# Kernel tuning notes

Measured on AMD Instinct MI355X. Metric: run time of the kernel, lower is better.

The kernel has to match this reference:

```python
import jax, jax.numpy as jnp
import numpy as np
from jax import lax

N_EXPERTS = 256
N_GROUP = 8
TOPK_GROUP = 4
TOP_K = 8
AUX_ALPHA = 0.001


def setup_inputs() -> dict:
    key = jax.random.key(0)
    k1, k2 = jax.random.split(key)
    hidden_states = jax.random.normal(k1, (16384, 2048), dtype=jnp.float32)
    weight = jax.random.normal(k2, (N_EXPERTS, 2048), dtype=jnp.float32) * 0.02
    return {"hidden_states": hidden_states, "weight": weight}


def reference(hidden_states, weight):
    n_tokens = hidden_states.shape[0]
    group_size = N_EXPERTS // N_GROUP  # 32

    # gating logits: [N, E]
    logits = jnp.einsum('nh,eh->ne', hidden_states, weight)

    # group-restricted top-k: [N, G, group_size] -> top TOPK_GROUP per group
    group_logits = logits.reshape(n_tokens, N_GROUP, group_size)
    gw, gi = lax.top_k(group_logits, TOPK_GROUP)          # [N, G, tg]
    gw = gw.reshape(n_tokens, N_GROUP * TOPK_GROUP)
    gi = gi.reshape(n_tokens, N_GROUP * TOPK_GROUP)

    # global top-k over the pooled group winners
    topk_weights, ti = lax.top_k(gw, TOP_K)               # [N, K]
    selected_group = ti // TOPK_GROUP
    expert_in_group = jnp.take_along_axis(gi, ti, axis=1)
    topk_idx = selected_group * group_size + expert_in_group  # [N, K]

    # norm_topk_prob=True
    topk_weights = topk_weights / (jnp.sum(topk_weights, axis=-1, keepdims=True) + 1e-20)

    # auxiliary load-balancing loss (training path)
    expert_mask = jax.nn.one_hot(topk_idx.reshape(-1), N_EXPERTS, dtype=jnp.float32)
    expert_counts = expert_mask.mean(axis=0)              # [E]
    expert_probs = jax.nn.softmax(logits, axis=-1).mean(axis=0)  # [E]
    aux_loss = jnp.sum(expert_counts * expert_probs) * AUX_ALPHA

    return topk_idx, topk_weights, aux_loss
```

## Files before the change

kernel.cpp:

```cpp
#include <hip/hip_runtime.h>
#include <math.h>

#define NTOK 16384
#define KD   2048
#define NE   256
#define BM   32
#define NSTEP 64
#define EPS  2.5e-4f

using bf16x8 = __attribute__((ext_vector_type(8))) short;
using f32x16 = __attribute__((ext_vector_type(16))) float;
using u16 = unsigned short;
using u32 = unsigned int;

__device__ __forceinline__ u16 f2bf(float x) {
    u32 u = __float_as_uint(x);
    return (u16)((u + 0x7FFFu + ((u >> 16) & 1u)) >> 16);
}
__device__ __forceinline__ float bf2f(u16 h) {
    return __uint_as_float(((u32)h) << 16);
}

__global__ __launch_bounds__(256) void wsplit_kernel(
    const float* __restrict__ wgt, u16* __restrict__ Whi, u16* __restrict__ Wlo)
{
    const int idx = blockIdx.x * 256 + threadIdx.x;
    const int e  = idx >> 8;
    const int ko = idx & 255;
    const int k  = ko * 8;
    const int c  = k >> 5, s = (k >> 4) & 1, kh = (k >> 3) & 1;
    const int dst = (c * 2 + s) * 4096 + (e >> 6) * 1024 + ((e >> 5) & 1) * 512
                  + kh * 256 + (e & 31) * 8;
    const float* p = wgt + (size_t)e * KD + k;
    u16 hi[8], lo[8];
#pragma unroll
    for (int i = 0; i < 8; ++i) {
        const float w = p[i];
        hi[i] = f2bf(w);
        lo[i] = f2bf(w - bf2f(hi[i]));
    }
    *(uint4*)(Whi + dst) = *(const uint4*)hi;
    *(uint4*)(Wlo + dst) = *(const uint4*)lo;
}

__global__ __launch_bounds__(256, 4) void gate_kernel(
    const float* __restrict__ hid, const u16* __restrict__ Whi, const u16* __restrict__ Wlo,
    float* __restrict__ out, float* __restrict__ cnt, float* __restrict__ prb,
    int* __restrict__ flagcnt, int* __restrict__ flaglist)
{
    __shared__ union {
        struct { u16 ah[2][BM][40]; u16 al[2][BM][40]; } st;
        float ls[BM][257];
    } sh;
    __shared__ float maxS[BM], sumS[BM], invS[BM];

    const int tid  = threadIdx.x;
    const int lane = tid & 63;
    const int wv   = tid >> 6;
    const int ln31 = lane & 31;
    const int kh8  = (lane >> 5) * 8;
    const int t0   = blockIdx.x * BM;

    f32x16 acc[2];
#pragma unroll
    for (int nf = 0; nf < 2; ++nf)
#pragma unroll
        for (int r = 0; r < 16; ++r) acc[nf][r] = 0.f;

    float4 areg;
    const int am = tid >> 3;
    const int ak = (tid & 7) * 4;

    auto loadA = [&](int c) {
        areg = *(const float4*)(hid + (size_t)(t0 + am) * KD + c * 32 + ak);
    };
    auto writeA = [&](int buf) {
        float f[4] = {areg.x, areg.y, areg.z, areg.w};
#pragma unroll
        for (int i = 0; i < 4; ++i) {
            const u16 hi = f2bf(f[i]);
            sh.st.ah[buf][am][ak + i] = hi;
            sh.st.al[buf][am][ak + i] = f2bf(f[i] - bf2f(hi));
        }
    };

    loadA(0); writeA(0);
    int cur = 0;

#pragma unroll 1
    for (int c = 0; c < NSTEP; ++c) {
        __syncthreads();
        const int nxt = cur ^ 1;
        if (c + 1 < NSTEP) loadA(c + 1);

        const u16* bbase = (const u16*)0;
#pragma unroll
        for (int s = 0; s < 2; ++s) {
            const int boff = (c * 2 + s) * 4096 + wv * 1024 + lane * 8;
            const bf16x8 bh0 = *(const bf16x8*)(Whi + boff);
            const bf16x8 bl0 = *(const bf16x8*)(Wlo + boff);
            const bf16x8 bh1 = *(const bf16x8*)(Whi + boff + 512);
            const bf16x8 bl1 = *(const bf16x8*)(Wlo + boff + 512);
            const bf16x8 ah  = *(const bf16x8*)&sh.st.ah[cur][ln31][s * 16 + kh8];
            const bf16x8 al  = *(const bf16x8*)&sh.st.al[cur][ln31][s * 16 + kh8];

            acc[0] = __builtin_amdgcn_mfma_f32_32x32x16_bf16(ah, bh0, acc[0], 0, 0, 0);
            acc[0] = __builtin_amdgcn_mfma_f32_32x32x16_bf16(ah, bl0, acc[0], 0, 0, 0);
            acc[0] = __builtin_amdgcn_mfma_f32_32x32x16_bf16(al, bh0, acc[0], 0, 0, 0);
            acc[1] = __builtin_amdgcn_mfma_f32_32x32x16_bf16(ah, bh1, acc[1], 0, 0, 0);
            acc[1] = __builtin_amdgcn_mfma_f32_32x32x16_bf16(ah, bl1, acc[1], 0, 0, 0);
            acc[1] = __builtin_amdgcn_mfma_f32_32x32x16_bf16(al, bh1, acc[1], 0, 0, 0);
        }
        (void)bbase;
        if (c + 1 < NSTEP) writeA(nxt);
        cur = nxt;
    }

    __syncthreads();
#pragma unroll
    for (int nf = 0; nf < 2; ++nf) {
        const int col = wv * 64 + nf * 32 + ln31;
#pragma unroll
        for (int r = 0; r < 16; ++r) {
            const int row = (r & 3) + 8 * (r >> 2) + 4 * (lane >> 5);
            sh.ls[row][col] = acc[nf][r];
        }
    }
    if (tid < BM) sumS[tid] = 0.f;
    __syncthreads();

    if (tid < BM) {
        const float* lr = &sh.ls[tid][0];
        float tv[9]; int ti[9];
#pragma unroll
        for (int j = 0; j < 9; ++j) { tv[j] = -1e30f; ti[j] = 0; }
        float gv3[8], gv4[8];
        float rowmax = -1e30f;

        auto ins9 = [&](float v, int idx) {
#pragma unroll
            for (int p = 0; p < 9; ++p) {
                if (v > tv[p]) {
#pragma unroll
                    for (int q = 8; q > p; --q) { tv[q] = tv[q - 1]; ti[q] = ti[q - 1]; }
                    tv[p] = v; ti[p] = idx;
                    break;
                }
            }
        };

#pragma unroll 1
        for (int g = 0; g < 8; ++g) {
            float v0 = -1e30f, v1 = -1e30f, v2 = -1e30f, v3 = -1e30f, v4 = -1e30f;
            int   i0 = 0, i1 = 0, i2 = 0, i3 = 0;
            for (int j = 0; j < 32; ++j) {
                const float v = lr[g * 32 + j];
                if (v > v0)      { v4=v3; v3=v2;i3=i2; v2=v1;i2=i1; v1=v0;i1=i0; v0=v;i0=j; }
                else if (v > v1) { v4=v3; v3=v2;i3=i2; v2=v1;i2=i1; v1=v;i1=j; }
                else if (v > v2) { v4=v3; v3=v2;i3=i2; v2=v;i2=j; }
                else if (v > v3) { v4=v3; v3=v;i3=j; }
                else if (v > v4) { v4=v; }
            }
            rowmax = fmaxf(rowmax, v0);
            gv3[g] = v3; gv4[g] = v4;
            ins9(v0, g * 32 + i0);
            ins9(v1, g * 32 + i1);
            ins9(v2, g * 32 + i2);
            ins9(v3, g * 32 + i3);
        }

        bool flag = false;
#pragma unroll
        for (int r = 0; r < 8; ++r)
            if (tv[r] - tv[r + 1] < EPS) flag = true;
#pragma unroll
        for (int g = 0; g < 8; ++g)
            if (gv3[g] - gv4[g] < EPS && gv3[g] > tv[7] - EPS) flag = true;

        const float s01 = __fadd_rn(tv[0], tv[1]);
        const float s23 = __fadd_rn(tv[2], tv[3]);
        const float s45 = __fadd_rn(tv[4], tv[5]);
        const float s67 = __fadd_rn(tv[6], tv[7]);
        float s = __fadd_rn(__fadd_rn(s01, s23), __fadd_rn(s45, s67));
        s = __fadd_rn(s, 1e-20f);

        const size_t tg2 = (size_t)(t0 + tid);
#pragma unroll
        for (int j = 0; j < 8; ++j) {
            out[tg2 * 8 + j]                    = (float)ti[j];
            out[(size_t)NTOK * 8 + tg2 * 8 + j] = __fdiv_rn(tv[j], s);
            atomicAdd(&cnt[ti[j]], 1.0f);
        }
        if (flag) {
            const int fi = atomicAdd(flagcnt, 1);
            flaglist[fi] = t0 + tid;
        }
        maxS[tid] = rowmax;
    }
    __syncthreads();

    {
        const int t  = tid >> 3;
        const int c0 = (tid & 7) * 32;
        const float m = maxS[t];
        float part = 0.f;
#pragma unroll
        for (int j = 0; j < 32; ++j) part += __expf(sh.ls[t][c0 + j] - m);
        atomicAdd(&sumS[t], part);
    }
    __syncthreads();
    if (tid < BM) invS[tid] = 1.0f / sumS[tid];
    __syncthreads();

    {
        float p = 0.f;
#pragma unroll
        for (int n = 0; n < BM; ++n) p += __expf(sh.ls[n][tid] - maxS[n]) * invS[n];
        atomicAdd(&prb[tid], p);
    }
}

__global__ __launch_bounds__(256) void exact_kernel(
    const float* __restrict__ hid, const float* __restrict__ wgt,
    float* __restrict__ out, float* __restrict__ cnt,
    const int* __restrict__ flagcnt, const int* __restrict__ flaglist)
{
    const int fn = *flagcnt;

    __shared__ float wch[256 * 17];
    __shared__ float hch[8 * 17];
    __shared__ float exls[8][257];
    __shared__ int tk[8];

    const int tid = threadIdx.x;
    const int tg  = tid >> 7;
    const int eg  = (tid >> 2) & 31;
    const int l   = tid & 3;

#pragma unroll 1
    for (int base = blockIdx.x * 8; base < fn; base += 64 * 8) {
        const int nt = min(8, fn - base);
        __syncthreads();
        if (tid < 8) tk[tid] = (tid < nt) ? flaglist[base + tid] : flaglist[base];
        __syncthreads();

        float accq[4][8];
#pragma unroll
        for (int i = 0; i < 4; ++i)
#pragma unroll
            for (int j = 0; j < 8; ++j) accq[i][j] = 0.f;

#pragma unroll 1
        for (int c = 0; c < 128; ++c) {
            __syncthreads();
            {
                const float* p = wgt + (size_t)tid * KD + c * 16;
                float4 w0 = *(const float4*)(p);
                float4 w1 = *(const float4*)(p + 4);
                float4 w2 = *(const float4*)(p + 8);
                float4 w3 = *(const float4*)(p + 12);
                float* wr = &wch[tid * 17];
                wr[0]=w0.x; wr[1]=w0.y; wr[2]=w0.z; wr[3]=w0.w;
                wr[4]=w1.x; wr[5]=w1.y; wr[6]=w1.z; wr[7]=w1.w;
                wr[8]=w2.x; wr[9]=w2.y; wr[10]=w2.z; wr[11]=w2.w;
                wr[12]=w3.x; wr[13]=w3.y; wr[14]=w3.z; wr[15]=w3.w;
            }
            if (tid < 128) {
                const int tok = tid >> 4, k = tid & 15;
                hch[tok * 17 + k] = hid[(size_t)tk[tok] * KD + c * 16 + k];
            }
            __syncthreads();

#pragma unroll
            for (int q = 3; q >= 0; --q) {
                const int k = 4 * q + l;
                float hv[4], wv2[8];
#pragma unroll
                for (int i = 0; i < 4; ++i) hv[i] = hch[(tg * 4 + i) * 17 + k];
#pragma unroll
                for (int j = 0; j < 8; ++j) wv2[j] = wch[(j * 32 + eg) * 17 + k];
#pragma unroll
                for (int i = 0; i < 4; ++i)
#pragma unroll
                    for (int j = 0; j < 8; ++j)
                        accq[i][j] = __fadd_rn(__fmul_rn(hv[i], wv2[j]), accq[i][j]);
            }
        }

        __syncthreads();
#pragma unroll
        for (int i = 0; i < 4; ++i)
#pragma unroll
            for (int j = 0; j < 8; ++j) {
                float v = accq[i][j];
                v = __fadd_rn(v, __shfl_xor(v, 1));
                v = __fadd_rn(v, __shfl_xor(v, 2));
                if (l == 0) exls[tg * 4 + i][j * 32 + eg] = v;
            }
        __syncthreads();

        if (tid < nt) {
            const float* lr = &exls[tid][0];
            float tv[8]; int ti[8];
#pragma unroll
            for (int j = 0; j < 8; ++j) { tv[j] = -1e30f; ti[j] = 0; }

            auto ins8 = [&](float v, int idx) {
#pragma unroll
                for (int p = 0; p < 8; ++p) {
                    if (v > tv[p]) {
#pragma unroll
                        for (int q = 7; q > p; --q) { tv[q] = tv[q - 1]; ti[q] = ti[q - 1]; }
                        tv[p] = v; ti[p] = idx;
                        break;
                    }
                }
            };

#pragma unroll 1
            for (int g = 0; g < 8; ++g) {
                float v0 = -1e30f, v1 = -1e30f, v2 = -1e30f, v3 = -1e30f;
                int   i0 = 0, i1 = 0, i2 = 0, i3 = 0;
                for (int j = 0; j < 32; ++j) {
                    const float v = lr[g * 32 + j];
                    if (v > v0)      { v3=v2;i3=i2; v2=v1;i2=i1; v1=v0;i1=i0; v0=v;i0=j; }
                    else if (v > v1) { v3=v2;i3=i2; v2=v1;i2=i1; v1=v;i1=j; }
                    else if (v > v2) { v3=v2;i3=i2; v2=v;i2=j; }
                    else if (v > v3) { v3=v;i3=j; }
                }
                ins8(v0, g * 32 + i0);
                ins8(v1, g * 32 + i1);
                ins8(v2, g * 32 + i2);
                ins8(v3, g * 32 + i3);
            }

            const float s01 = __fadd_rn(tv[0], tv[1]);
            const float s23 = __fadd_rn(tv[2], tv[3]);
            const float s45 = __fadd_rn(tv[4], tv[5]);
            const float s67 = __fadd_rn(tv[6], tv[7]);
            float s = __fadd_rn(__fadd_rn(s01, s23), __fadd_rn(s45, s67));
            s = __fadd_rn(s, 1e-20f);

            const size_t gt = (size_t)tk[tid];
#pragma unroll
            for (int j = 0; j < 8; ++j) {
                const int oldi = (int)out[gt * 8 + j];
                if (oldi != ti[j]) {
                    atomicAdd(&cnt[oldi], -1.0f);
                    atomicAdd(&cnt[ti[j]], 1.0f);
                }
                out[gt * 8 + j]                    = (float)ti[j];
                out[(size_t)NTOK * 8 + gt * 8 + j] = __fdiv_rn(tv[j], s);
            }
        }
        __syncthreads();
    }
}

__global__ void aux_kernel(const float* __restrict__ cnt,
                           const float* __restrict__ prb,
                           float* __restrict__ out)
{
    const int tid = threadIdx.x;
    float v = cnt[tid] * prb[tid];
#pragma unroll
    for (int off = 32; off; off >>= 1) v += __shfl_down(v, off, 64);
    __shared__ float ps[4];
    if ((tid & 63) == 0) ps[tid >> 6] = v;
    __syncthreads();
    if (tid == 0) {
        const float tot = ps[0] + ps[1] + ps[2] + ps[3];
        out[(size_t)NTOK * 8 * 2] = tot * (0.001f / (131072.0f * 16384.0f));
    }
}

extern "C" void kernel_launch(void* const* d_in, const int* in_sizes, int n_in,
                              void* d_out, int out_size, void* d_ws, size_t ws_size,
                              hipStream_t stream)
{
    (void)in_sizes; (void)n_in; (void)out_size; (void)ws_size;
    const float* hid = (const float*)d_in[0];
    const float* wgt = (const float*)d_in[1];
    float* out = (float*)d_out;

    float* cnt      = (float*)d_ws;
    float* prb      = cnt + NE;
    int*   flagcnt  = (int*)(prb + NE);
    int*   flaglist = flagcnt + 64;
    u16*   Whi      = (u16*)(flaglist + NTOK);
    u16*   Wlo      = Whi + (size_t)NE * KD;

    hipMemsetAsync(d_ws, 0, (2 * NE + 64) * sizeof(float), stream);
    wsplit_kernel<<<NE * KD / 8 / 256, 256, 0, stream>>>(wgt, Whi, Wlo);
    gate_kernel<<<NTOK / BM, 256, 0, stream>>>(hid, Whi, Wlo, out, cnt, prb, flagcnt, flaglist);
    exact_kernel<<<64, 256, 0, stream>>>(hid, wgt, out, cnt, flagcnt, flaglist);
    aux_kernel<<<1, 256, 0, stream>>>(cnt, prb, out);
}
```

Baseline: 493.2 us.

## Register double-buffer weight fragments and unroll gate GEMM loop by two

The gate GEMM loop now prefetches the next chunk's bf16 hi/lo weight fragments into a second register set before issuing the current chunk's MFMAs. The loop is unrolled by two with fixed shared-memory buffer indices, so global weight loads overlap with matrix math rather than being issued and consumed back to back. The occupancy hint in launch_bounds is dropped so the compiler can use more registers for the extra fragments, which may reduce waves per CU. The exact kernel's grid stride now uses gridDim.x instead of a hardcoded 64.

```diff
diff --git a/kernel.cpp b/kernel.cpp
--- a/kernel.cpp
+++ b/kernel.cpp
@@ -43,7 +43,9 @@
     *(uint4*)(Wlo + dst) = *(const uint4*)lo;
 }
 
-__global__ __launch_bounds__(256, 4) void gate_kernel(
+#define MFMA32(A, B, C) __builtin_amdgcn_mfma_f32_32x32x16_bf16((A), (B), (C), 0, 0, 0)
+
+__global__ __launch_bounds__(256) void gate_kernel(
     const float* __restrict__ hid, const u16* __restrict__ Whi, const u16* __restrict__ Wlo,
     float* __restrict__ out, float* __restrict__ cnt, float* __restrict__ prb,
     int* __restrict__ flagcnt, int* __restrict__ flaglist)
@@ -84,39 +86,65 @@
         }
     };
 
-    loadA(0); writeA(0);
-    int cur = 0;
+    const u16* bwh = Whi + wv * 1024 + lane * 8;
+    const u16* bwl = Wlo + wv * 1024 + lane * 8;
+
+    bf16x8 p0h0, p0l0, p0h1, p0l1, p0h2, p0l2, p0h3, p0l3;
+    bf16x8 p1h0, p1l0, p1h1, p1l1, p1h2, p1l2, p1h3, p1l3;
+
+#define LOADB(P, cc) do {                                           \
+    const u16* _ph = bwh + (cc) * 8192;                             \
+    const u16* _pl = bwl + (cc) * 8192;                             \
+    P##h0 = *(const bf16x8*)(_ph);                                  \
+    P##l0 = *(const bf16x8*)(_pl);                                  \
+    P##h1 = *(const bf16x8*)(_ph + 512);                            \
+    P##l1 = *(const bf16x8*)(_pl + 512);                            \
+    P##h2 = *(const bf16x8*)(_ph + 4096);                           \
+    P##l2 = *(const bf16x8*)(_pl + 4096);                           \
+    P##h3 = *(const bf16x8*)(_ph + 4608);                           \
+    P##l3 = *(const bf16x8*)(_pl + 4608);                           \
+} while (0)
+
+#define COMPUTE(P, CUR) do {                                        \
+    bf16x8 ah0 = *(const bf16x8*)&sh.st.ah[CUR][ln31][kh8];         \
+    bf16x8 al0 = *(const bf16x8*)&sh.st.al[CUR][ln31][kh8];         \
+    acc[0] = MFMA32(ah0, P##h0, acc[0]);                            \
+    acc[0] = MFMA32(ah0, P##l0, acc[0]);                            \
+    acc[0] = MFMA32(al0, P##h0, acc[0]);                            \
+    acc[1] = MFMA32(ah0, P##h1, acc[1]);                            \
+    acc[1] = MFMA32(ah0, P##l1, acc[1]);                            \
+    acc[1] = MFMA32(al0, P##h1, acc[1]);                            \
+    bf16x8 ah1 = *(const bf16x8*)&sh.st.ah[CUR][ln31][16 + kh8];    \
+    bf16x8 al1 = *(const bf16x8*)&sh.st.al[CUR][ln31][16 + kh8];    \
+    acc[0] = MFMA32(ah1, P##h2, acc[0]);                            \
+    acc[0] = MFMA32(ah1, P##l2, acc[0]);                            \
+    acc[0] = MFMA32(al1, P##h2, acc[0]);                            \
+    acc[1] = MFMA32(ah1, P##h3, acc[1]);                            \
+    acc[1] = MFMA32(ah1, P##l3, acc[1]);                            \
+    acc[1] = MFMA32(al1, P##h3, acc[1]);                            \
+} while (0)
+
+    loadA(0);
+    writeA(0);
+    LOADB(p0, 0);
+    __syncthreads();
 
 #pragma unroll 1
-    for (int c = 0; c < NSTEP; ++c) {
-        __syncthreads();
-        const int nxt = cur ^ 1;
-        if (c + 1 < NSTEP) loadA(c + 1);
-
-        const u16* bbase = (const u16*)0;
-#pragma unroll
-        for (int s = 0; s < 2; ++s) {
-            const int boff = (c * 2 + s) * 4096 + wv * 1024 + lane * 8;
-            const bf16x8 bh0 = *(const bf16x8*)(Whi + boff);
-            const bf16x8 bl0 = *(const bf16x8*)(Wlo + boff);
-            const bf16x8 bh1 = *(const bf16x8*)(Whi + boff + 512);
-            const bf16x8 bl1 = *(const bf16x8*)(Wlo + boff + 512);
-            const bf16x8 ah  = *(const bf16x8*)&sh.st.ah[cur][ln31][s * 16 + kh8];
-            const bf16x8 al  = *(const bf16x8*)&sh.st.al[cur][ln31][s * 16 + kh8];
-
-            acc[0] = __builtin_amdgcn_mfma_f32_32x32x16_bf16(ah, bh0, acc[0], 0, 0, 0);
-            acc[0] = __builtin_amdgcn_mfma_f32_32x32x16_bf16(ah, bl0, acc[0], 0, 0, 0);
-            acc[0] = __builtin_amdgcn_mfma_f32_32x32x16_bf16(al, bh0, acc[0], 0, 0, 0);
-            acc[1] = __builtin_amdgcn_mfma_f32_32x32x16_bf16(ah, bh1, acc[1], 0, 0, 0);
-            acc[1] = __builtin_amdgcn_mfma_f32_32x32x16_bf16(ah, bl1, acc[1], 0, 0, 0);
-            acc[1] = __builtin_amdgcn_mfma_f32_32x32x16_bf16(al, bh1, acc[1], 0, 0, 0);
-        }
-        (void)bbase;
-        if (c + 1 < NSTEP) writeA(nxt);
-        cur = nxt;
-    }
-
-    __syncthreads();
+    for (int c = 0; c < NSTEP; c += 2) {
+        loadA(c + 1);
+        LOADB(p1, c + 1);
+        COMPUTE(p0, 0);
+        writeA(1);
+        __syncthreads();
+        if (c + 2 < NSTEP) {
+            loadA(c + 2);
+            LOADB(p0, c + 2);
+        }
+        COMPUTE(p1, 1);
+        if (c + 2 < NSTEP) writeA(0);
+        __syncthreads();
+    }
+
 #pragma unroll
     for (int nf = 0; nf < 2; ++nf) {
         const int col = wv * 64 + nf * 32 + ln31;
@@ -238,7 +266,7 @@
     const int l   = tid & 3;
 
 #pragma unroll 1
-    for (int base = blockIdx.x * 8; base < fn; base += 64 * 8) {
+    for (int base = blockIdx.x * 8; base < fn; base += gridDim.x * 8) {
         const int nt = min(8, fn - base);
         __syncthreads();
         if (tid < 8) tk[tid] = (tid < nt) ? flaglist[base + tid] : flaglist[base];
```

Result: no change. 486.5 us (-1.4%).

## Stage gate weights into LDS via async global_load_lds, widen exact_kernel grid

Applied to the files above, without the earlier changes.

The gate GEMM previously had every wave read its bf16 hi/lo weight fragments straight from global memory on each K step. It now double-buffers a full 32-column K slab of both weight splits in shared memory using global_load_lds, prefetching the next slab while the current one feeds the MFMAs. Separately, the exact-recompute kernel now launches 256 blocks instead of 64, with a grid-stride loop based on gridDim. The costs are much larger LDS use per block (about 64KB for the B buffers) and a dropped occupancy hint in launch_bounds, so fewer blocks can be resident per CU.

```diff
diff --git a/kernel.cpp b/kernel.cpp
--- a/kernel.cpp
+++ b/kernel.cpp
@@ -43,15 +43,24 @@
     *(uint4*)(Wlo + dst) = *(const uint4*)lo;
 }
 
-__global__ __launch_bounds__(256, 4) void gate_kernel(
+typedef __attribute__((address_space(1))) const void GV;
+typedef __attribute__((address_space(3))) void LV;
+__device__ __forceinline__ void gld_lds16(const void* g, void* l) {
+    __builtin_amdgcn_global_load_lds((GV*)g, (LV*)l, 16, 0, 0);
+}
+
+#define MFMA32(A, B, C) __builtin_amdgcn_mfma_f32_32x32x16_bf16((A), (B), (C), 0, 0, 0)
+
+__global__ __launch_bounds__(256) void gate_kernel(
     const float* __restrict__ hid, const u16* __restrict__ Whi, const u16* __restrict__ Wlo,
     float* __restrict__ out, float* __restrict__ cnt, float* __restrict__ prb,
     int* __restrict__ flagcnt, int* __restrict__ flaglist)
 {
     __shared__ union {
-        struct { u16 ah[2][BM][40]; u16 al[2][BM][40]; } st;
+        struct { u16 bh[2][8192]; u16 bl[2][8192]; } st;
         float ls[BM][257];
     } sh;
+    __shared__ u16 ah[2][BM][40], al[2][BM][40];
     __shared__ float maxS[BM], sumS[BM], invS[BM];
 
     const int tid  = threadIdx.x;
@@ -79,39 +88,48 @@
 #pragma unroll
         for (int i = 0; i < 4; ++i) {
             const u16 hi = f2bf(f[i]);
-            sh.st.ah[buf][am][ak + i] = hi;
-            sh.st.al[buf][am][ak + i] = f2bf(f[i] - bf2f(hi));
+            ah[buf][am][ak + i] = hi;
+            al[buf][am][ak + i] = f2bf(f[i] - bf2f(hi));
         }
     };
-
-    loadA(0); writeA(0);
+    auto stageB = [&](int c, int buf) {
+        const u16* srch = Whi + (size_t)c * 8192 + tid * 8;
+        const u16* srcl = Wlo + (size_t)c * 8192 + tid * 8;
+        u16* dsth = &sh.st.bh[buf][tid * 8];
+        u16* dstl = &sh.st.bl[buf][tid * 8];
+#pragma unroll
+        for (int seg = 0; seg < 4; ++seg) {
+            gld_lds16(srch + seg * 2048, dsth + seg * 2048);
+            gld_lds16(srcl + seg * 2048, dstl + seg * 2048);
+        }
+    };
+
+    loadA(0); stageB(0, 0); writeA(0);
     int cur = 0;
 
 #pragma unroll 1
     for (int c = 0; c < NSTEP; ++c) {
         __syncthreads();
         const int nxt = cur ^ 1;
-        if (c + 1 < NSTEP) loadA(c + 1);
-
-        const u16* bbase = (const u16*)0;
+        if (c + 1 < NSTEP) { loadA(c + 1); stageB(c + 1, nxt); }
+
 #pragma unroll
         for (int s = 0; s < 2; ++s) {
-            const int boff = (c * 2 + s) * 4096 + wv * 1024 + lane * 8;
-            const bf16x8 bh0 = *(const bf16x8*)(Whi + boff);
-            const bf16x8 bl0 = *(const bf16x8*)(Wlo + boff);
-            const bf16x8 bh1 = *(const bf16x8*)(Whi + boff + 512);
-            const bf16x8 bl1 = *(const bf16x8*)(Wlo + boff + 512);
-            const bf16x8 ah  = *(const bf16x8*)&sh.st.ah[cur][ln31][s * 16 + kh8];
-            const bf16x8 al  = *(const bf16x8*)&sh.st.al[cur][ln31][s * 16 + kh8];
-
-            acc[0] = __builtin_amdgcn_mfma_f32_32x32x16_bf16(ah, bh0, acc[0], 0, 0, 0);
-            acc[0] = __builtin_amdgcn_mfma_f32_32x32x16_bf16(ah, bl0, acc[0], 0, 0, 0);
-            acc[0] = __builtin_amdgcn_mfma_f32_32x32x16_bf16(al, bh0, acc[0], 0, 0, 0);
-            acc[1] = __builtin_amdgcn_mfma_f32_32x32x16_bf16(ah, bh1, acc[1], 0, 0, 0);
-            acc[1] = __builtin_amdgcn_mfma_f32_32x32x16_bf16(ah, bl1, acc[1], 0, 0, 0);
-            acc[1] = __builtin_amdgcn_mfma_f32_32x32x16_bf16(al, bh1, acc[1], 0, 0, 0);
-        }
-        (void)bbase;
+            const int boff = s * 4096 + wv * 1024 + lane * 8;
+            const bf16x8 bh0 = *(const bf16x8*)&sh.st.bh[cur][boff];
+            const bf16x8 bl0 = *(const bf16x8*)&sh.st.bl[cur][boff];
+            const bf16x8 bh1 = *(const bf16x8*)&sh.st.bh[cur][boff + 512];
+            const bf16x8 bl1 = *(const bf16x8*)&sh.st.bl[cur][boff + 512];
+            const bf16x8 a_h = *(const bf16x8*)&ah[cur][ln31][s * 16 + kh8];
+            const bf16x8 a_l = *(const bf16x8*)&al[cur][ln31][s * 16 + kh8];
+
+            acc[0] = MFMA32(a_h, bh0, acc[0]);
+            acc[0] = MFMA32(a_h, bl0, acc[0]);
+            acc[0] = MFMA32(a_l, bh0, acc[0]);
+            acc[1] = MFMA32(a_h, bh1, acc[1]);
+            acc[1] = MFMA32(a_h, bl1, acc[1]);
+            acc[1] = MFMA32(a_l, bh1, acc[1]);
+        }
         if (c + 1 < NSTEP) writeA(nxt);
         cur = nxt;
     }
@@ -238,7 +256,7 @@
     const int l   = tid & 3;
 
 #pragma unroll 1
-    for (int base = blockIdx.x * 8; base < fn; base += 64 * 8) {
+    for (int base = blockIdx.x * 8; base < fn; base += gridDim.x * 8) {
         const int nt = min(8, fn - base);
         __syncthreads();
         if (tid < 8) tk[tid] = (tid < nt) ? flaglist[base + tid] : flaglist[base];
@@ -393,6 +411,6 @@
     hipMemsetAsync(d_ws, 0, (2 * NE + 64) * sizeof(float), stream);
     wsplit_kernel<<<NE * KD / 8 / 256, 256, 0, stream>>>(wgt, Whi, Wlo);
     gate_kernel<<<NTOK / BM, 256, 0, stream>>>(hid, Whi, Wlo, out, cnt, prb, flagcnt, flaglist);
-    exact_kernel<<<64, 256, 0, stream>>>(hid, wgt, out, cnt, flagcnt, flaglist);
+    exact_kernel<<<256, 256, 0, stream>>>(hid, wgt, out, cnt, flagcnt, flaglist);
     aux_kernel<<<1, 256, 0, stream>>>(cnt, prb, out);
 }
```

Measured after the change: 516.5 us. +4.7%, slower.

## Switch split-precision gate GEMM from bf16 to scaled fp16 with 512-thread blocks

Applied to the files above, without the earlier changes.

Replaces the bf16 hi/lo split with an fp16 hi plus a 2048-scaled fp16 lo residual. The extra precision lets the near-tie flag threshold EPS shrink, so fewer tokens should go through the slow exact fp32 recompute. The gate kernel now runs 8 waves per block, each owning 32 experts with separate hi and lo accumulators, which removes the dependent MFMA chain per accumulator. The exact kernel grid grows from 64 to 1024 blocks and uses a grid-stride loop to spread the flagged tokens wider. Risks are fp16 overflow or underflow on outliers and lower occupancy from the larger blocks.

```diff
diff --git a/kernel.cpp b/kernel.cpp
--- a/kernel.cpp
+++ b/kernel.cpp
@@ -6,19 +6,15 @@
 #define NE   256
 #define BM   32
 #define NSTEP 64
-#define EPS  2.5e-4f
-
-using bf16x8 = __attribute__((ext_vector_type(8))) short;
+#define EPS  5e-5f
+
+using halfx8 = __attribute__((ext_vector_type(8))) _Float16;
 using f32x16 = __attribute__((ext_vector_type(16))) float;
 using u16 = unsigned short;
 using u32 = unsigned int;
 
-__device__ __forceinline__ u16 f2bf(float x) {
-    u32 u = __float_as_uint(x);
-    return (u16)((u + 0x7FFFu + ((u >> 16) & 1u)) >> 16);
-}
-__device__ __forceinline__ float bf2f(u16 h) {
-    return __uint_as_float(((u32)h) << 16);
+__device__ __forceinline__ u16 h2u(_Float16 h) {
+    union { _Float16 h; u16 u; } v; v.h = h; return v.u;
 }
 
 __global__ __launch_bounds__(256) void wsplit_kernel(
@@ -29,21 +25,23 @@
     const int ko = idx & 255;
     const int k  = ko * 8;
     const int c  = k >> 5, s = (k >> 4) & 1, kh = (k >> 3) & 1;
-    const int dst = (c * 2 + s) * 4096 + (e >> 6) * 1024 + ((e >> 5) & 1) * 512
-                  + kh * 256 + (e & 31) * 8;
+    const int dst = (c * 2 + s) * 4096 + (e >> 5) * 512 + kh * 256 + (e & 31) * 8;
     const float* p = wgt + (size_t)e * KD + k;
     u16 hi[8], lo[8];
 #pragma unroll
     for (int i = 0; i < 8; ++i) {
         const float w = p[i];
-        hi[i] = f2bf(w);
-        lo[i] = f2bf(w - bf2f(hi[i]));
+        const _Float16 h = (_Float16)w;
+        const _Float16 l = (_Float16)((w - (float)h) * 2048.0f);
+        hi[i] = h2u(h); lo[i] = h2u(l);
     }
     *(uint4*)(Whi + dst) = *(const uint4*)hi;
     *(uint4*)(Wlo + dst) = *(const uint4*)lo;
 }
 
-__global__ __launch_bounds__(256, 4) void gate_kernel(
+#define MFMA16(A, B, C) __builtin_amdgcn_mfma_f32_32x32x16_f16((A), (B), (C), 0, 0, 0)
+
+__global__ __launch_bounds__(512) void gate_kernel(
     const float* __restrict__ hid, const u16* __restrict__ Whi, const u16* __restrict__ Wlo,
     float* __restrict__ out, float* __restrict__ cnt, float* __restrict__ prb,
     int* __restrict__ flagcnt, int* __restrict__ flaglist)
@@ -58,29 +56,28 @@
     const int lane = tid & 63;
     const int wv   = tid >> 6;
     const int ln31 = lane & 31;
-    const int kh8  = (lane >> 5) * 8;
+    const int kh   = lane >> 5;
     const int t0   = blockIdx.x * BM;
 
-    f32x16 acc[2];
-#pragma unroll
-    for (int nf = 0; nf < 2; ++nf)
-#pragma unroll
-        for (int r = 0; r < 16; ++r) acc[nf][r] = 0.f;
-
-    float4 areg;
-    const int am = tid >> 3;
-    const int ak = (tid & 7) * 4;
+    f32x16 accH, accL;
+#pragma unroll
+    for (int r = 0; r < 16; ++r) { accH[r] = 0.f; accL[r] = 0.f; }
+
+    float2 areg;
+    const int am = tid >> 4;
+    const int ak = (tid & 15) * 2;
 
     auto loadA = [&](int c) {
-        areg = *(const float4*)(hid + (size_t)(t0 + am) * KD + c * 32 + ak);
+        areg = *(const float2*)(hid + (size_t)(t0 + am) * KD + c * 32 + ak);
     };
     auto writeA = [&](int buf) {
-        float f[4] = {areg.x, areg.y, areg.z, areg.w};
-#pragma unroll
-        for (int i = 0; i < 4; ++i) {
-            const u16 hi = f2bf(f[i]);
-            sh.st.ah[buf][am][ak + i] = hi;
-            sh.st.al[buf][am][ak + i] = f2bf(f[i] - bf2f(hi));
+        const float f[2] = {areg.x, areg.y};
+#pragma unroll
+        for (int i = 0; i < 2; ++i) {
+            const _Float16 h = (_Float16)f[i];
+            const _Float16 l = (_Float16)((f[i] - (float)h) * 2048.0f);
+            sh.st.ah[buf][am][ak + i] = h2u(h);
+            sh.st.al[buf][am][ak + i] = h2u(l);
         }
     };
 
@@ -93,37 +90,28 @@
         const int nxt = cur ^ 1;
         if (c + 1 < NSTEP) loadA(c + 1);
 
-        const u16* bbase = (const u16*)0;
 #pragma unroll
         for (int s = 0; s < 2; ++s) {
-            const int boff = (c * 2 + s) * 4096 + wv * 1024 + lane * 8;
-            const bf16x8 bh0 = *(const bf16x8*)(Whi + boff);
-            const bf16x8 bl0 = *(const bf16x8*)(Wlo + boff);
-            const bf16x8 bh1 = *(const bf16x8*)(Whi + boff + 512);
-            const bf16x8 bl1 = *(const bf16x8*)(Wlo + boff + 512);
-            const bf16x8 ah  = *(const bf16x8*)&sh.st.ah[cur][ln31][s * 16 + kh8];
-            const bf16x8 al  = *(const bf16x8*)&sh.st.al[cur][ln31][s * 16 + kh8];
-
-            acc[0] = __builtin_amdgcn_mfma_f32_32x32x16_bf16(ah, bh0, acc[0], 0, 0, 0);
-            acc[0] = __builtin_amdgcn_mfma_f32_32x32x16_bf16(ah, bl0, acc[0], 0, 0, 0);
-            acc[0] = __builtin_amdgcn_mfma_f32_32x32x16_bf16(al, bh0, acc[0], 0, 0, 0);
-            acc[1] = __builtin_amdgcn_mfma_f32_32x32x16_bf16(ah, bh1, acc[1], 0, 0, 0);
-            acc[1] = __builtin_amdgcn_mfma_f32_32x32x16_bf16(ah, bl1, acc[1], 0, 0, 0);
-            acc[1] = __builtin_amdgcn_mfma_f32_32x32x16_bf16(al, bh1, acc[1], 0, 0, 0);
-        }
-        (void)bbase;
+            const halfx8 a_h = *(const halfx8*)&sh.st.ah[cur][ln31][s * 16 + kh * 8];
+            const halfx8 a_l = *(const halfx8*)&sh.st.al[cur][ln31][s * 16 + kh * 8];
+            const int bo = (c * 2 + s) * 4096 + wv * 512 + kh * 256 + ln31 * 8;
+            const halfx8 bh = *(const halfx8*)(Whi + bo);
+            const halfx8 bl = *(const halfx8*)(Wlo + bo);
+            accH = MFMA16(a_h, bh, accH);
+            accL = MFMA16(a_h, bl, accL);
+            accL = MFMA16(a_l, bh, accL);
+        }
         if (c + 1 < NSTEP) writeA(nxt);
         cur = nxt;
     }
 
     __syncthreads();
-#pragma unroll
-    for (int nf = 0; nf < 2; ++nf) {
-        const int col = wv * 64 + nf * 32 + ln31;
+    {
+        const int col = wv * 32 + ln31;
 #pragma unroll
         for (int r = 0; r < 16; ++r) {
-            const int row = (r & 3) + 8 * (r >> 2) + 4 * (lane >> 5);
-            sh.ls[row][col] = acc[nf][r];
+            const int row = (r & 3) + 8 * (r >> 2) + 4 * kh;
+            sh.ls[row][col] = accH[r] + accL[r] * (1.0f / 2048.0f);
         }
     }
     if (tid < BM) sumS[tid] = 0.f;
@@ -200,21 +188,21 @@
     __syncthreads();
 
     {
-        const int t  = tid >> 3;
-        const int c0 = (tid & 7) * 32;
+        const int t  = tid >> 4;
+        const int c0 = (tid & 15) * 16;
         const float m = maxS[t];
         float part = 0.f;
 #pragma unroll
-        for (int j = 0; j < 32; ++j) part += __expf(sh.ls[t][c0 + j] - m);
+        for (int j = 0; j < 16; ++j) part += __expf(sh.ls[t][c0 + j] - m);
         atomicAdd(&sumS[t], part);
     }
     __syncthreads();
     if (tid < BM) invS[tid] = 1.0f / sumS[tid];
     __syncthreads();
 
-    {
+    if (tid < NE) {
         float p = 0.f;
-#pragma unroll
+#pragma unroll 4
         for (int n = 0; n < BM; ++n) p += __expf(sh.ls[n][tid] - maxS[n]) * invS[n];
         atomicAdd(&prb[tid], p);
     }
@@ -238,7 +226,7 @@
     const int l   = tid & 3;
 
 #pragma unroll 1
-    for (int base = blockIdx.x * 8; base < fn; base += 64 * 8) {
+    for (int base = blockIdx.x * 8; base < fn; base += gridDim.x * 8) {
         const int nt = min(8, fn - base);
         __syncthreads();
         if (tid < 8) tk[tid] = (tid < nt) ? flaglist[base + tid] : flaglist[base];
@@ -392,7 +380,7 @@
 
     hipMemsetAsync(d_ws, 0, (2 * NE + 64) * sizeof(float), stream);
     wsplit_kernel<<<NE * KD / 8 / 256, 256, 0, stream>>>(wgt, Whi, Wlo);
-    gate_kernel<<<NTOK / BM, 256, 0, stream>>>(hid, Whi, Wlo, out, cnt, prb, flagcnt, flaglist);
-    exact_kernel<<<64, 256, 0, stream>>>(hid, wgt, out, cnt, flagcnt, flaglist);
+    gate_kernel<<<NTOK / BM, 512, 0, stream>>>(hid, Whi, Wlo, out, cnt, prb, flagcnt, flaglist);
+    exact_kernel<<<1024, 256, 0, stream>>>(hid, wgt, out, cnt, flagcnt, flaglist);
     aux_kernel<<<1, 256, 0, stream>>>(cnt, prb, out);
 }
```

New measurement: 527.4 us. 1.07x slower.
